# Performance work log

Measured on AMD Instinct MI355X. Metric: run time of the kernel, lower is better.

Reference implementation:

```python
import jax, jax.numpy as jnp
import numpy as np

NUM_PHRASES = 24
TOPN = 32
N = NUM_PHRASES * TOPN  # 768 graph nodes (phrase-box candidates)
D = 1024                # visual_dim
NUM_PAIRS = 24          # connected phrase pairs -> E = NUM_PAIRS * TOPN^2 = 24576 edges
STEPS = 1               # cfg.MODEL.RELATION.VISUAL_GRAPH_PASSING_TIME


def _build_graph():
    """Deterministic sparse connectivity: edges between all boxes of connected phrase pairs,
    ordered row-major like np.where(conn_map >= 0) in the original."""
    rng = np.random.default_rng(0)
    pairs = set()
    while len(pairs) < NUM_PAIRS:
        p1, p2 = rng.integers(0, NUM_PHRASES, size=2)
        if p1 != p2:
            pairs.add((int(p1), int(p2)))
    pairs = sorted(pairs)
    sbj_list, obj_list = [], []
    for p1, p2 in pairs:
        s = np.arange(TOPN) + p1 * TOPN
        o = np.arange(TOPN) + p2 * TOPN
        ss, oo = np.meshgrid(s, o, indexing='ij')
        sbj_list.append(ss.ravel())
        obj_list.append(oo.ravel())
    sbj = np.concatenate(sbj_list)
    obj = np.concatenate(obj_list)
    order = np.lexsort((obj, sbj))  # np.where row-major order
    sbj, obj = sbj[order], obj[order]
    involved = np.zeros(N, dtype=bool)
    for p1, p2 in pairs:
        involved[p1 * TOPN:(p1 + 1) * TOPN] = True
        involved[p2 * TOPN:(p2 + 1) * TOPN] = True
    return sbj.astype(np.int32), obj.astype(np.int32), involved


def setup_inputs() -> dict:
    sbj, obj, involved = _build_graph()
    E = sbj.shape[0]
    key = jax.random.key(0)
    ks = jax.random.split(key, 8)
    def w(k, shape, fan_in):
        return jax.random.normal(k, shape, dtype=jnp.float32) / np.float32(np.sqrt(fan_in))
    zD = jnp.zeros((D,), jnp.float32)
    return {
        "visual_feat": jax.random.normal(ks[0], (N, D), jnp.float32),
        "rel_visual_feat": jax.random.normal(ks[1], (E, D), jnp.float32),
        "W_rel": w(ks[2], (3 * D, D), 3 * D), "b_rel": zD,
        "W_sbj": w(ks[3], (2 * D, D), 2 * D), "b_sbj": zD,
        "W_obj": w(ks[4], (2 * D, D), 2 * D), "b_obj": zD,
        "W_ctx": w(ks[5], (D, D), D), "b_ctx": zD,
        "sbj_ind": jnp.asarray(sbj),
        "obj_ind": jnp.asarray(obj),
        "involved_mask": jnp.asarray(involved),
    }


def _edge_softmax(logits, seg, num_segments):
    # masked softmax over the sparse connectivity, normalized per segment (row or column)
    m = jax.ops.segment_max(logits, seg, num_segments=num_segments)
    e = jnp.exp(logits - m[seg])
    s = jax.ops.segment_sum(e, seg, num_segments=num_segments)
    return e / s[seg]


def reference(visual_feat, rel_visual_feat, W_rel, b_rel, W_sbj, b_sbj,
              W_obj, b_obj, W_ctx, b_ctx, sbj_ind, obj_ind, involved_mask):
    n, d = visual_feat.shape
    scale = np.float32(1.0 / np.sqrt(d))
    # split concat-Linear weights so we never materialize [E, 3D]/[E, 2D] concats
    Wr_s, Wr_o, Wr_r = W_rel[:d], W_rel[d:2 * d], W_rel[2 * d:]
    Ws_v, Ws_r = W_sbj[:d], W_sbj[d:]
    Wo_v, Wo_r = W_obj[:d], W_obj[d:]
    vj = visual_feat
    for _ in range(STEPS):
        vs = vj[sbj_ind]          # [E, D] gather
        vo = vj[obj_ind]          # [E, D] gather
        rel = vs @ Wr_s + vo @ Wr_o + rel_visual_feat @ Wr_r + b_rel  # rel_update_embedding
        ts = vs @ Ws_v + rel @ Ws_r + b_sbj   # visual_joint_trans_sbj
        to = vo @ Wo_v + rel @ Wo_r + b_obj   # visual_joint_trans_obj
        logits = jnp.sum(ts * to, axis=1) * scale  # [E]
        w_sbj = _edge_softmax(logits, sbj_ind, n)  # softmax over dim=1 (per subject row)
        w_obj = _edge_softmax(logits, obj_ind, n)  # softmax over dim=0 (per object col)
        # ctx[i] = sum_j w_sbj[i,j] * vj[j] + sum_j w_obj[j,i] * vj[j]  (sparse scatter-add)
        ctx = jax.ops.segment_sum(w_sbj[:, None] * vo, sbj_ind, num_segments=n) \
            + jax.ops.segment_sum(w_obj[:, None] * vs, obj_ind, num_segments=n)
        upd = vj + ctx @ W_ctx + b_ctx  # residual + visual_ctx_embedding, involved nodes only
        vj = jnp.where(involved_mask[:, None], upd, vj)
    return (rel_visual_feat, vj)
```

## Files before the change

kernel.cpp:

```cpp
#include <hip/hip_runtime.h>
#include <hip/hip_bf16.h>
#include <math.h>
#include <type_traits>

typedef __bf16 v8bf __attribute__((ext_vector_type(8)));
typedef __bf16 v4bf __attribute__((ext_vector_type(4)));
typedef float  v4f  __attribute__((ext_vector_type(4)));

__device__ __forceinline__ float wave_reduce_sum(float v) {
#pragma unroll
    for (int m = 1; m < 64; m <<= 1) v += __shfl_xor(v, m, 64);
    return v;
}

__device__ __forceinline__ unsigned fenc(float x) {
    unsigned u = __float_as_uint(x);
    return (u & 0x80000000u) ? ~u : (u | 0x80000000u);
}
__device__ __forceinline__ float fdec(unsigned k) {
    return (k & 0x80000000u) ? __uint_as_float(k ^ 0x80000000u) : __uint_as_float(~k);
}

__device__ __forceinline__ void gload16(const void* g, void* l) {
    __builtin_amdgcn_global_load_lds((const __attribute__((address_space(1))) void*)g,
                                     (__attribute__((address_space(3))) void*)l, 16, 0, 0);
}


__global__ __launch_bounds__(256) void cvt_f32_bf16(const float* __restrict__ in,
                                                    __bf16* __restrict__ out, long long n) {
    long long i = ((long long)blockIdx.x * 256 + threadIdx.x) * 4;
    if (i >= n) return;
    v4f v = *(const v4f*)(in + i);
    v4bf o;
    o[0] = (__bf16)v[0]; o[1] = (__bf16)v[1]; o[2] = (__bf16)v[2]; o[3] = (__bf16)v[3];
    *(v4bf*)(out + i) = o;
}

__global__ __launch_bounds__(256) void copy_cvt(const float* __restrict__ in,
                                                float* __restrict__ outCopy,
                                                __bf16* __restrict__ outB, long long n) {
    long long i = ((long long)blockIdx.x * 256 + threadIdx.x) * 4;
    if (i >= n) return;
    v4f v = *(const v4f*)(in + i);
    *(v4f*)(outCopy + i) = v;
    v4bf o;
    o[0] = (__bf16)v[0]; o[1] = (__bf16)v[1]; o[2] = (__bf16)v[2]; o[3] = (__bf16)v[3];
    *(v4bf*)(outB + i) = o;
}

__global__ __launch_bounds__(256) void cvt_t_bf16(const float* __restrict__ in,
                                                  __bf16* __restrict__ out, int R, int C) {
    __shared__ float tile[32][33];
    int cb = blockIdx.x * 32, rb = blockIdx.y * 32;
    int tx = threadIdx.x & 31, ty = threadIdx.x >> 5;
#pragma unroll
    for (int i = 0; i < 32; i += 8)
        tile[ty + i][tx] = in[(size_t)(rb + ty + i) * C + cb + tx];
    __syncthreads();
#pragma unroll
    for (int i = 0; i < 32; i += 8)
        out[(size_t)(cb + ty + i) * R + rb + tx] = (__bf16)tile[tx][ty + i];
}

template <int MODE, bool BIG>
__global__ __launch_bounds__(256, 4) void gemm_gl(
    const __bf16* __restrict__ Ap, int ldA,
    const __bf16* __restrict__ Btp, int ldB,
    int M, int N, int K,
    long zA, long zB, long zOut,
    const float* __restrict__ addMat, int ldAdd,
    float* __restrict__ outF,
    __bf16* __restrict__ outB, int ldOut,
    __bf16* __restrict__ outB2,
    const __bf16* __restrict__ rbDot,
    float* __restrict__ qOut,
    const float* __restrict__ addRow,
    const int* __restrict__ maskRow,
    const int* __restrict__ sbjI,
    const int* __restrict__ objI) {
    constexpr int BM = BIG ? 128 : 64;
    constexpr int BN = BIG ? 128 : 64;
    constexpr int WM = BM / 2, WN = BN / 2;
    constexpr int FI = WM / 16, FJ = WN / 16;
    constexpr int NLA = (BM * 64) / 2048;
    constexpr int NLB = (BN * 64) / 2048;

    __shared__ alignas(16) __bf16 As[BM * 64];
    __shared__ alignas(16) __bf16 Bs[BN * 64];

    Ap  += zA * (long)blockIdx.z;
    Btp += zB * (long)blockIdx.z;
    outF += zOut * (long)blockIdx.z;

    const int m0 = blockIdx.x * BM, n0 = blockIdx.y * BN;
    const int t = threadIdx.x, lane = t & 63, wid = t >> 6;
    const int wm = wid >> 1, wn = wid & 1;
    const int rA = t >> 3;
    const int cSw = (t & 7) ^ (rA & 7);

    v4f acc[FI][FJ] = {};

    const int l15 = lane & 15;
    const int xorMask = (l15 & 7) << 4;

    for (int kt = 0; kt < K; kt += 64) {
#pragma unroll
        for (int i = 0; i < NLA; ++i)
            gload16(Ap + (size_t)(m0 + i * 32 + rA) * ldA + kt + cSw * 8,
                    (char*)As + i * 4096 + wid * 1024);
#pragma unroll
        for (int i = 0; i < NLB; ++i)
            gload16(Btp + (size_t)(n0 + i * 32 + rA) * ldB + kt + cSw * 8,
                    (char*)Bs + i * 4096 + wid * 1024);
        __syncthreads();
#pragma unroll
        for (int ks = 0; ks < 2; ++ks) {
            const int kb = (ks * 64 + ((lane >> 4) << 4)) ^ xorMask;
            v8bf af[FI], bfr[FJ];
#pragma unroll
            for (int f = 0; f < FI; ++f)
                af[f] = *(const v8bf*)((const char*)As + (wm * WM + f * 16 + l15) * 128 + kb);
#pragma unroll
            for (int f = 0; f < FJ; ++f)
                bfr[f] = *(const v8bf*)((const char*)Bs + (wn * WN + f * 16 + l15) * 128 + kb);
#pragma unroll
            for (int i = 0; i < FI; ++i)
#pragma unroll
                for (int j = 0; j < FJ; ++j)
                    acc[i][j] = __builtin_amdgcn_mfma_f32_16x16x32_bf16(af[i], bfr[j], acc[i][j], 0, 0, 0);
        }
        __syncthreads();
    }

    const int cc = lane & 15, r4 = (lane >> 4) << 2;
    if constexpr (MODE == 3) {
#pragma unroll
        for (int i = 0; i < FI; ++i)
#pragma unroll
            for (int r = 0; r < 4; ++r) {
                const int gm = m0 + wm * WM + i * 16 + r4 + r;
                const int s = sbjI[gm], o = objI[gm];
                const float* Ps = addMat + (size_t)s * ldAdd;
                const float* Qo = outF + (size_t)o * ldAdd;
                float p = 0.f;
#pragma unroll
                for (int j = 0; j < FJ; ++j) {
                    const int gn = n0 + wn * WN + j * 16 + cc;
                    float rv = (float)rbDot[(size_t)gm * N + gn];
                    p += rv * (acc[i][j][r] + Ps[gn] + Qo[gn] + addRow[gn]);
                }
                p += __shfl_xor(p, 1, 64);
                p += __shfl_xor(p, 2, 64);
                p += __shfl_xor(p, 4, 64);
                p += __shfl_xor(p, 8, 64);
                if (cc == 0) atomicAdd(qOut + gm, p);
            }
    } else if constexpr (MODE == 5) {
        const int mb = m0 >> 10, nb = n0 >> 10;
        const size_t DDe = (size_t)ldOut * ldOut;
#pragma unroll
        for (int i = 0; i < FI; ++i)
#pragma unroll
            for (int j = 0; j < FJ; ++j)
#pragma unroll
                for (int r = 0; r < 4; ++r) {
                    const int gm = m0 + wm * WM + i * 16 + r4 + r;
                    const int gn = n0 + wn * WN + j * 16 + cc;
                    const int gml = gm & 1023, gnl = gn & 1023;
                    float v = acc[i][j][r];
                    if (mb == 2) {
                        outB2[(size_t)gml * 2048 + gn] = (__bf16)v;
                    } else {
                        int blk;
                        if (mb == 0) { blk = nb ? 0 : 1; if (nb) v += addMat[(size_t)gml * ldAdd + gnl]; }
                        else         { blk = nb ? 2 : 3; if (!nb) v += addRow[(size_t)gml * ldAdd + gnl]; }
                        outB[blk * DDe + (size_t)gnl * ldOut + gml] = (__bf16)v;
                    }
                }
    } else {
#pragma unroll
        for (int i = 0; i < FI; ++i)
#pragma unroll
            for (int j = 0; j < FJ; ++j)
#pragma unroll
                for (int r = 0; r < 4; ++r) {
                    const int gm = m0 + wm * WM + i * 16 + r4 + r;
                    const int gn = n0 + wn * WN + j * 16 + cc;
                    float v = acc[i][j][r];
                    if constexpr (MODE == 0) {
                        if (addMat) v += addMat[(size_t)gm * ldAdd + gn];
                        outB[(size_t)gm * ldOut + gn] = (__bf16)v;
                    } else if constexpr (MODE == 2) {
                        outF[(size_t)gm * ldOut + gn] = v;
                    } else {
                        float u = addMat[(size_t)gm * ldAdd + gn];
                        if (maskRow[gm]) u += v + addRow[gn];
                        outF[(size_t)gm * ldOut + gn] = u;
                    }
                }
    }
}


__global__ __launch_bounds__(256) void beta_kernel(
    const float* __restrict__ b_rel, const float* __restrict__ b_sbj, const float* __restrict__ b_obj,
    const float* __restrict__ Wsr, const float* __restrict__ Wor,
    float* __restrict__ bs, float* __restrict__ bo, int D, int rowsPerChunk) {
    const int col = blockIdx.x * 256 + threadIdx.x;
    if (col >= D) return;
    const int r0 = blockIdx.y * rowsPerChunk;
    const float* W = (blockIdx.z == 0) ? Wsr : Wor;
    float acc = 0.f;
    if (blockIdx.y == 0) acc = (blockIdx.z == 0) ? b_sbj[col] : b_obj[col];
    const int rEnd = min(r0 + rowsPerChunk, D);
    for (int r = r0; r < rEnd; ++r)
        acc += b_rel[r] * W[(size_t)r * D + col];
    float* out = (blockIdx.z == 0) ? bs : bo;
    atomicAdd(out + col, acc);
}

__global__ __launch_bounds__(256) void pbeta_kernel(const float* __restrict__ bs,
                                                    const float* __restrict__ bo,
                                                    const __bf16* __restrict__ KoKs,
                                                    float* __restrict__ pb, int D) {
    int d = blockIdx.x * 4 + (threadIdx.x >> 6);
    int lane = threadIdx.x & 63;
    float a = 0.f;
    for (int j = lane; j < D; j += 64)
        a += bs[j] * (float)KoKs[(size_t)d * 2048 + j] + bo[j] * (float)KoKs[(size_t)d * 2048 + 1024 + j];
    a = wave_reduce_sum(a);
    if (lane == 0) pb[d] = a;
}

__global__ __launch_bounds__(256) void node_kernel(
    const __bf16* __restrict__ ACBD,
    const float* __restrict__ bs, const float* __restrict__ bo,
    float* __restrict__ nodeS, float* __restrict__ nodeO, int D) {
    int n = blockIdx.x * 4 + (threadIdx.x >> 6);
    int lane = threadIdx.x & 63;
    int d0 = lane * 16;
    const __bf16* row = ACBD + (size_t)n * 4 * D;
    const __bf16* pa = row + d0;
    const __bf16* pc = row + D + d0;
    const __bf16* pB = row + 2 * D + d0;
    const __bf16* pd = row + 3 * D + d0;
    float s1 = 0.f, s2 = 0.f;
#pragma unroll
    for (int u = 0; u < 16; ++u) {
        float a = (float)pa[u], c = (float)pc[u], b = (float)pB[u], dd = (float)pd[u];
        float vs_ = bs[d0 + u], vo_ = bo[d0 + u];
        s1 += a * c + a * vo_ + vs_ * c;
        s2 += b * dd + b * vo_ + vs_ * dd;
    }
    s1 = wave_reduce_sum(s1);
    s2 = wave_reduce_sum(s2);
    if (lane == 0) { nodeS[n] = s1; nodeO[n] = s2; }
}

__global__ __launch_bounds__(256) void edge_scalar_kernel(
    const float* __restrict__ q,
    const float* __restrict__ nodeS, const float* __restrict__ nodeO,
    const float* __restrict__ G_AD, const float* __restrict__ G_BC,
    const int* __restrict__ sbj, const int* __restrict__ obj,
    float* __restrict__ logits, int E, int Nn, float scale) {
    int e = blockIdx.x * 256 + threadIdx.x;
    if (e >= E) return;
    int s = sbj[e], o = obj[e];
    logits[e] = (q[e] + nodeS[s] + nodeO[o] +
                 G_AD[(size_t)s * Nn + o] + G_BC[(size_t)o * Nn + s]) * scale;
}

__global__ __launch_bounds__(256) void segmax_kernel(const float* __restrict__ logits,
                                                     const int* __restrict__ sbj,
                                                     const int* __restrict__ obj,
                                                     unsigned* __restrict__ mS,
                                                     unsigned* __restrict__ mO, int E) {
    int e = blockIdx.x * 256 + threadIdx.x;
    if (e >= E) return;
    unsigned k = fenc(logits[e]);
    atomicMax(mS + sbj[e], k);
    atomicMax(mO + obj[e], k);
}

__global__ __launch_bounds__(256) void expsum_kernel(const float* __restrict__ logits,
                                                     const int* __restrict__ sbj,
                                                     const int* __restrict__ obj,
                                                     const unsigned* __restrict__ mS,
                                                     const unsigned* __restrict__ mO,
                                                     float* __restrict__ es, float* __restrict__ eo,
                                                     float* __restrict__ sumS, float* __restrict__ sumO,
                                                     int E) {
    int e = blockIdx.x * 256 + threadIdx.x;
    if (e >= E) return;
    float l = logits[e];
    int s = sbj[e], o = obj[e];
    float a = expf(l - fdec(mS[s]));
    es[e] = a;
    atomicAdd(sumS + s, a);
    float b = expf(l - fdec(mO[o]));
    eo[e] = b;
    atomicAdd(sumO + o, b);
}

__global__ __launch_bounds__(256) void scatter_kernel(const float* __restrict__ es,
                                                      const float* __restrict__ eo,
                                                      const float* __restrict__ sumS,
                                                      const float* __restrict__ sumO,
                                                      const int* __restrict__ sbj,
                                                      const int* __restrict__ obj,
                                                      float* __restrict__ S, int* __restrict__ inv,
                                                      int E, int Nn) {
    int e = blockIdx.x * 256 + threadIdx.x;
    if (e >= E) return;
    int s = sbj[e], o = obj[e];
    atomicAdd(S + (size_t)s * Nn + o, es[e] / sumS[s]);
    atomicAdd(S + (size_t)o * Nn + s, eo[e] / sumO[o]);
    inv[s] = 1;
    inv[o] = 1;
}


extern "C" void kernel_launch(void* const* d_in, const int* in_sizes, int n_in,
                              void* d_out, int out_size, void* d_ws, size_t ws_size,
                              hipStream_t stream) {
    const float* V     = (const float*)d_in[0];
    const float* relv  = (const float*)d_in[1];
    const float* W_rel = (const float*)d_in[2];
    const float* b_rel = (const float*)d_in[3];
    const float* W_sbj = (const float*)d_in[4];
    const float* b_sbj = (const float*)d_in[5];
    const float* W_obj = (const float*)d_in[6];
    const float* b_obj = (const float*)d_in[7];
    const float* W_ctx = (const float*)d_in[8];
    const float* b_ctx = (const float*)d_in[9];
    const int* sbj = (const int*)d_in[10];
    const int* obj = (const int*)d_in[11];

    const int D  = in_sizes[3];
    const int E  = in_sizes[10];
    const int Nn = in_sizes[12];
    const size_t DD = (size_t)D * D;

    const float* Ws_v = W_sbj;
    const float* Ws_r = W_sbj + DD;
    const float* Wo_v = W_obj;
    const float* Wo_r = W_obj + DD;

    char* ws = (char*)d_ws;
    size_t off = 0;
    auto alloc = [&](size_t bytes) -> void* {
        void* p = (void*)(ws + off);
        off += (bytes + 255) & ~(size_t)255;
        return p;
    };

    __bf16* relv_b = (__bf16*)alloc((size_t)E * D * 2);
    __bf16* Vb     = (__bf16*)alloc((size_t)Nn * D * 2);
    __bf16* VbT    = (__bf16*)alloc((size_t)D * Nn * 2);
    __bf16* ZT_b   = (__bf16*)alloc(DD * 2);
    __bf16* KoKs   = (__bf16*)alloc((size_t)D * 2 * D * 2);
    __bf16* ACBD   = (__bf16*)alloc((size_t)Nn * 4 * D * 2);
    size_t r1 = off;
    __bf16* Wr_all = (__bf16*)(ws + r1);
    float*  G_AD   = (float*)(ws + r1);
    float*  G_BC   = G_AD + (size_t)Nn * Nn;
    {
        size_t a = 3 * DD * 2, b = 2 * (size_t)Nn * Nn * 4;
        off += ((a > b ? a : b) + 255) & ~(size_t)255;
    }
    size_t r2 = off;
    __bf16* WoWs_T = (__bf16*)(ws + r2);
    __bf16* W_ctxT = (__bf16*)(ws + r2);
    off += 2 * DD * 2;
    size_t r3 = off;
    __bf16* MT_all = (__bf16*)(ws + r3);
    float*  Pm     = (float*)(ws + r3);
    float*  Qm     = Pm + (size_t)Nn * D;
    {
        size_t a = 4 * DD * 2, b = 2 * (size_t)Nn * D * 4;
        off += ((a > b ? a : b) + 255) & ~(size_t)255;
    }
    float* pb     = (float*)alloc((size_t)D * 4);
    float* nodeS  = (float*)alloc((size_t)Nn * 4);
    float* nodeO  = (float*)alloc((size_t)Nn * 4);
    float* logits = (float*)alloc((size_t)E * 4);
    float* es     = (float*)alloc((size_t)E * 4);
    float* eo     = (float*)alloc((size_t)E * 4);
    size_t zbeg = off;
    float* S      = (float*)alloc((size_t)Nn * Nn * 4);
    float* q      = (float*)alloc((size_t)E * 4);
    float* bs     = (float*)alloc((size_t)D * 4);
    float* bo     = (float*)alloc((size_t)D * 4);
    unsigned* mS  = (unsigned*)alloc((size_t)Nn * 4);
    unsigned* mO  = (unsigned*)alloc((size_t)Nn * 4);
    float* sumS   = (float*)alloc((size_t)Nn * 4);
    float* sumO   = (float*)alloc((size_t)Nn * 4);
    int* inv      = (int*)alloc((size_t)Nn * 4);
    size_t zend = off;
    __bf16* Sb    = (__bf16*)alloc((size_t)Nn * Nn * 2);
    __bf16* ctx_b = (__bf16*)alloc((size_t)Nn * D * 2);
    (void)ws_size; (void)n_in; (void)out_size;

    float* outVj = (float*)d_out + (size_t)E * D;

    hipMemsetAsync(ws + zbeg, 0, zend - zbeg, stream);

    auto cvt = [&](const float* in, __bf16* out, size_t n) {
        int blocks = (int)((n / 4 + 255) / 256);
        cvt_f32_bf16<<<dim3(blocks), dim3(256), 0, stream>>>(in, out, (long long)n);
    };
    auto cvtT = [&](const float* in, __bf16* out, int R, int C) {
        cvt_t_bf16<<<dim3(C / 32, R / 32), dim3(256), 0, stream>>>(in, out, R, C);
    };
    {
        long long n = (long long)E * D;
        copy_cvt<<<dim3((int)(n / 4 / 256)), dim3(256), 0, stream>>>(relv, (float*)d_out, relv_b, n);
    }
    cvt(W_rel, Wr_all, 3 * DD);
    cvt(V, Vb, (size_t)Nn * D);
    cvtT(Wo_r, WoWs_T, D, D);
    cvtT(Ws_r, WoWs_T + DD, D, D);
    cvtT(V, VbT, Nn, D);

    beta_kernel<<<dim3((D + 255) / 256, 32, 2), dim3(256), 0, stream>>>(
        b_rel, b_sbj, b_obj, Ws_r, Wo_r, bs, bo, D, (D + 31) / 32);

    auto G = [&](auto modeTag, auto bigTag, const __bf16* A, int ldA, const __bf16* Bt, int ldB,
                 int M, int N2, int K, int nz, long zA, long zB, long zOut,
                 const float* addMat, int ldAdd, float* outF, __bf16* outB, int ldOut,
                 __bf16* outB2, const __bf16* rbD, float* qO, const float* addRow, const int* mask,
                 const int* sbjI = nullptr, const int* objI = nullptr) {
        constexpr int BT = decltype(bigTag)::value ? 128 : 64;
        gemm_gl<decltype(modeTag)::value, decltype(bigTag)::value>
            <<<dim3(M / BT, N2 / BT, nz), dim3(256), 0, stream>>>(
                A, ldA, Bt, ldB, M, N2, K, zA, zB, zOut, addMat, ldAdd, outF, outB, ldOut,
                outB2, rbD, qO, addRow, mask, sbjI, objI);
    };
    using M0 = std::integral_constant<int, 0>;
    using M2 = std::integral_constant<int, 2>;
    using M3 = std::integral_constant<int, 3>;
    using M4 = std::integral_constant<int, 4>;
    using M5 = std::integral_constant<int, 5>;
    using SMALL = std::integral_constant<bool, false>;
    using LARGE = std::integral_constant<bool, true>;

    G(M5{}, LARGE{}, Wr_all, D, WoWs_T, D, 3 * D, 2 * D, D, 1, 0, 0, 0,
      Ws_v, D, nullptr, MT_all, D, KoKs, nullptr, nullptr, Wo_v, nullptr);
    cvtT(W_ctx, W_ctxT, D, D);
    G(M0{}, SMALL{}, KoKs + 0, 2 * D, KoKs + D, 2 * D, D, D, D, 1, 0, 0, 0,
      nullptr, 0, nullptr, ZT_b, D, nullptr, nullptr, nullptr, nullptr, nullptr);
    pbeta_kernel<<<dim3(D / 4), dim3(256), 0, stream>>>(bs, bo, KoKs, pb, D);

    G(M0{}, SMALL{}, Vb, D, MT_all, D, Nn, 4 * D, D, 1, 0, 0, 0,
      nullptr, 0, nullptr, ACBD, 4 * D, nullptr, nullptr, nullptr, nullptr, nullptr);

    G(M2{}, SMALL{}, ACBD + 0 * D, 4 * D, ACBD + 3 * D, 4 * D, Nn, Nn, D, 2,
      2 * (long)D, -2 * (long)D, (long)Nn * Nn,
      nullptr, 0, G_AD, nullptr, Nn, nullptr, nullptr, nullptr, nullptr, nullptr);
    G(M2{}, SMALL{}, ACBD + 0 * D, 4 * D, KoKs, 2 * D, Nn, D, 2 * D, 2,
      2 * (long)D, 0, (long)Nn * D,
      nullptr, 0, Pm, nullptr, D, nullptr, nullptr, nullptr, nullptr, nullptr);

    node_kernel<<<dim3(Nn / 4), dim3(256), 0, stream>>>(ACBD, bs, bo, nodeS, nodeO, D);

    G(M3{}, LARGE{}, relv_b, D, ZT_b, D, E, D, D, 1, 0, 0, 0,
      Pm, D, Qm, nullptr, 0, nullptr, relv_b, q, pb, nullptr, sbj, obj);

    edge_scalar_kernel<<<dim3(E / 256), dim3(256), 0, stream>>>(
        q, nodeS, nodeO, G_AD, G_BC, sbj, obj, logits, E, Nn, 1.0f / sqrtf((float)D));
    segmax_kernel<<<dim3(E / 256), dim3(256), 0, stream>>>(logits, sbj, obj, mS, mO, E);
    expsum_kernel<<<dim3(E / 256), dim3(256), 0, stream>>>(logits, sbj, obj, mS, mO, es, eo, sumS, sumO, E);
    scatter_kernel<<<dim3(E / 256), dim3(256), 0, stream>>>(es, eo, sumS, sumO, sbj, obj, S, inv, E, Nn);

    cvt(S, Sb, (size_t)Nn * Nn);
    G(M0{}, SMALL{}, Sb, Nn, VbT, Nn, Nn, D, Nn, 1, 0, 0, 0,
      nullptr, 0, nullptr, ctx_b, D, nullptr, nullptr, nullptr, nullptr, nullptr);
    G(M4{}, SMALL{}, ctx_b, D, W_ctxT, D, Nn, D, D, 1, 0, 0, 0,
      V, D, outVj, nullptr, D, nullptr, nullptr, nullptr, b_ctx, inv);
}
```

Baseline: 380.4 us.

## Restructure weight-product GEMM to write contiguous outputs and fuse edge logit with segmax

The weight-combination GEMM now runs with transposed operands, so each output block is stored row-contiguously instead of through a transposed scatter. The additive terms come from newly transposed bf16 copies of Ws_v and Wo_v, produced by a batched four-way transpose kernel. The Wr_r product, which used to be handled as a third row block, moves to its own GEMM. Separately, the edge logit kernel now also performs the segment-max atomics, removing one kernel launch and one pass over the logits. The trade-off is two extra transposed weight buffers and one extra GEMM launch.

```diff
diff --git a/kernel.cpp b/kernel.cpp
--- a/kernel.cpp
+++ b/kernel.cpp
@@ -61,6 +61,25 @@
 #pragma unroll
     for (int i = 0; i < 32; i += 8)
         out[(size_t)(cb + ty + i) * R + rb + tx] = (__bf16)tile[tx][ty + i];
+}
+
+__global__ __launch_bounds__(256) void cvt_t4_bf16(
+    const float* __restrict__ in0, __bf16* __restrict__ out0,
+    const float* __restrict__ in1, __bf16* __restrict__ out1,
+    const float* __restrict__ in2, __bf16* __restrict__ out2,
+    const float* __restrict__ in3, __bf16* __restrict__ out3, int Dd) {
+    __shared__ float tile[32][33];
+    const float* in = (blockIdx.z == 0) ? in0 : (blockIdx.z == 1) ? in1 : (blockIdx.z == 2) ? in2 : in3;
+    __bf16* out = (blockIdx.z == 0) ? out0 : (blockIdx.z == 1) ? out1 : (blockIdx.z == 2) ? out2 : out3;
+    int cb = blockIdx.x * 32, rb = blockIdx.y * 32;
+    int tx = threadIdx.x & 31, ty = threadIdx.x >> 5;
+#pragma unroll
+    for (int i = 0; i < 32; i += 8)
+        tile[ty + i][tx] = in[(size_t)(rb + ty + i) * Dd + cb + tx];
+    __syncthreads();
+#pragma unroll
+    for (int i = 0; i < 32; i += 8)
+        out[(size_t)(cb + ty + i) * Dd + rb + tx] = (__bf16)tile[tx][ty + i];
 }
 
 template <int MODE, bool BIG>
@@ -156,27 +175,23 @@
                 p += __shfl_xor(p, 8, 64);
                 if (cc == 0) atomicAdd(qOut + gm, p);
             }
-    } else if constexpr (MODE == 5) {
+    } else if constexpr (MODE == 6) {
         const int mb = m0 >> 10, nb = n0 >> 10;
+        const int blk = (mb == 0) ? (nb ? 3 : 1) : (nb ? 2 : 0);
+        const __bf16* addB = (blk == 0) ? rbDot : (blk == 3 ? outB2 : nullptr);
         const size_t DDe = (size_t)ldOut * ldOut;
+        __bf16* dst = outB + (size_t)blk * DDe;
 #pragma unroll
         for (int i = 0; i < FI; ++i)
 #pragma unroll
             for (int j = 0; j < FJ; ++j)
 #pragma unroll
                 for (int r = 0; r < 4; ++r) {
-                    const int gm = m0 + wm * WM + i * 16 + r4 + r;
-                    const int gn = n0 + wn * WN + j * 16 + cc;
-                    const int gml = gm & 1023, gnl = gn & 1023;
+                    const int gml = (m0 + wm * WM + i * 16 + r4 + r) & 1023;
+                    const int gnl = (n0 + wn * WN + j * 16 + cc) & 1023;
                     float v = acc[i][j][r];
-                    if (mb == 2) {
-                        outB2[(size_t)gml * 2048 + gn] = (__bf16)v;
-                    } else {
-                        int blk;
-                        if (mb == 0) { blk = nb ? 0 : 1; if (nb) v += addMat[(size_t)gml * ldAdd + gnl]; }
-                        else         { blk = nb ? 2 : 3; if (!nb) v += addRow[(size_t)gml * ldAdd + gnl]; }
-                        outB[blk * DDe + (size_t)gnl * ldOut + gml] = (__bf16)v;
-                    }
+                    if (addB) v += (float)addB[(size_t)gml * ldOut + gnl];
+                    dst[(size_t)gml * ldOut + gnl] = (__bf16)v;
                 }
     } else {
 #pragma unroll
@@ -258,29 +273,22 @@
     if (lane == 0) { nodeS[n] = s1; nodeO[n] = s2; }
 }
 
-__global__ __launch_bounds__(256) void edge_scalar_kernel(
+__global__ __launch_bounds__(256) void edge_lmax_kernel(
     const float* __restrict__ q,
     const float* __restrict__ nodeS, const float* __restrict__ nodeO,
     const float* __restrict__ G_AD, const float* __restrict__ G_BC,
     const int* __restrict__ sbj, const int* __restrict__ obj,
-    float* __restrict__ logits, int E, int Nn, float scale) {
+    float* __restrict__ logits, unsigned* __restrict__ mS, unsigned* __restrict__ mO,
+    int E, int Nn, float scale) {
     int e = blockIdx.x * 256 + threadIdx.x;
     if (e >= E) return;
     int s = sbj[e], o = obj[e];
-    logits[e] = (q[e] + nodeS[s] + nodeO[o] +
-                 G_AD[(size_t)s * Nn + o] + G_BC[(size_t)o * Nn + s]) * scale;
-}
-
-__global__ __launch_bounds__(256) void segmax_kernel(const float* __restrict__ logits,
-                                                     const int* __restrict__ sbj,
-                                                     const int* __restrict__ obj,
-                                                     unsigned* __restrict__ mS,
-                                                     unsigned* __restrict__ mO, int E) {
-    int e = blockIdx.x * 256 + threadIdx.x;
-    if (e >= E) return;
-    unsigned k = fenc(logits[e]);
-    atomicMax(mS + sbj[e], k);
-    atomicMax(mO + obj[e], k);
+    float l = (q[e] + nodeS[s] + nodeO[o] +
+               G_AD[(size_t)s * Nn + o] + G_BC[(size_t)o * Nn + s]) * scale;
+    logits[e] = l;
+    unsigned k = fenc(l);
+    atomicMax(mS + s, k);
+    atomicMax(mO + o, k);
 }
 
 __global__ __launch_bounds__(256) void expsum_kernel(const float* __restrict__ logits,
@@ -361,6 +369,8 @@
     __bf16* ZT_b   = (__bf16*)alloc(DD * 2);
     __bf16* KoKs   = (__bf16*)alloc((size_t)D * 2 * D * 2);
     __bf16* ACBD   = (__bf16*)alloc((size_t)Nn * 4 * D * 2);
+    __bf16* Ws_vT  = (__bf16*)alloc(DD * 2);
+    __bf16* Wo_vT  = (__bf16*)alloc(DD * 2);
     size_t r1 = off;
     __bf16* Wr_all = (__bf16*)(ws + r1);
     float*  G_AD   = (float*)(ws + r1);
@@ -419,8 +429,8 @@
     }
     cvt(W_rel, Wr_all, 3 * DD);
     cvt(V, Vb, (size_t)Nn * D);
-    cvtT(Wo_r, WoWs_T, D, D);
-    cvtT(Ws_r, WoWs_T + DD, D, D);
+    cvt_t4_bf16<<<dim3(D / 32, D / 32, 4), dim3(256), 0, stream>>>(
+        Wo_r, WoWs_T, Ws_r, WoWs_T + DD, Ws_v, Ws_vT, Wo_v, Wo_vT, D);
     cvtT(V, VbT, Nn, D);
 
     beta_kernel<<<dim3((D + 255) / 256, 32, 2), dim3(256), 0, stream>>>(
@@ -441,12 +451,14 @@
     using M2 = std::integral_constant<int, 2>;
     using M3 = std::integral_constant<int, 3>;
     using M4 = std::integral_constant<int, 4>;
-    using M5 = std::integral_constant<int, 5>;
+    using M6 = std::integral_constant<int, 6>;
     using SMALL = std::integral_constant<bool, false>;
     using LARGE = std::integral_constant<bool, true>;
 
-    G(M5{}, LARGE{}, Wr_all, D, WoWs_T, D, 3 * D, 2 * D, D, 1, 0, 0, 0,
-      Ws_v, D, nullptr, MT_all, D, KoKs, nullptr, nullptr, Wo_v, nullptr);
+    G(M6{}, LARGE{}, WoWs_T, D, Wr_all, D, 2 * D, 2 * D, D, 1, 0, 0, 0,
+      nullptr, 0, nullptr, MT_all, D, Wo_vT, Ws_vT, nullptr, nullptr, nullptr);
+    G(M0{}, LARGE{}, Wr_all + 2 * DD, D, WoWs_T, D, D, 2 * D, D, 1, 0, 0, 0,
+      nullptr, 0, nullptr, KoKs, 2 * D, nullptr, nullptr, nullptr, nullptr, nullptr);
     cvtT(W_ctx, W_ctxT, D, D);
     G(M0{}, SMALL{}, KoKs + 0, 2 * D, KoKs + D, 2 * D, D, D, D, 1, 0, 0, 0,
       nullptr, 0, nullptr, ZT_b, D, nullptr, nullptr, nullptr, nullptr, nullptr);
@@ -467,9 +479,8 @@
     G(M3{}, LARGE{}, relv_b, D, ZT_b, D, E, D, D, 1, 0, 0, 0,
       Pm, D, Qm, nullptr, 0, nullptr, relv_b, q, pb, nullptr, sbj, obj);
 
-    edge_scalar_kernel<<<dim3(E / 256), dim3(256), 0, stream>>>(
-        q, nodeS, nodeO, G_AD, G_BC, sbj, obj, logits, E, Nn, 1.0f / sqrtf((float)D));
-    segmax_kernel<<<dim3(E / 256), dim3(256), 0, stream>>>(logits, sbj, obj, mS, mO, E);
+    edge_lmax_kernel<<<dim3(E / 256), dim3(256), 0, stream>>>(
+        q, nodeS, nodeO, G_AD, G_BC, sbj, obj, logits, mS, mO, E, Nn, 1.0f / sqrtf((float)D));
     expsum_kernel<<<dim3(E / 256), dim3(256), 0, stream>>>(logits, sbj, obj, mS, mO, es, eo, sumS, sumO, E);
     scatter_kernel<<<dim3(E / 256), dim3(256), 0, stream>>>(es, eo, sumS, sumO, sbj, obj, S, inv, E, Nn);
 
```

Measured after the change: 374.0 us. About the same (-1.7%).
